# Optimization experiments

Measured on AMD Instinct MI355X. Metric: run time of the kernel, lower is better.

The kernel has to match this reference:

```python
import jax, jax.numpy as jnp
import numpy as np

B, N, R, E = 4, 50000, 100000, 1_600_000   # batch, nodes (wavelets_col), wavelets_row, nnz
D_IN, H1, H2, D_OUT = 32, 32, 16, 1
NEG_SLOPE = 0.2


def _xavier(k, shape):
    lim = float(np.sqrt(6.0 / (shape[0] + shape[1])))
    return jax.random.uniform(k, shape, jnp.float32, -lim, lim)


def setup_inputs() -> dict:
    key = jax.random.key(0)
    ks = jax.random.split(key, 16)
    # wavelets: sparse (R x N); inverse wavelets: sparse (N x R)
    w_rows = jax.random.randint(ks[0], (E,), 0, R)
    w_cols = jax.random.randint(ks[1], (E,), 0, N)
    wi_rows = jax.random.randint(ks[2], (E,), 0, N)
    wi_cols = jax.random.randint(ks[3], (E,), 0, R)
    return {
        "wavelets_indices": jnp.stack([w_rows, w_cols]),
        "wavelets_values": jax.random.normal(ks[4], (E,), jnp.float32) * 0.05,
        "wavelets_inverse_indices": jnp.stack([wi_rows, wi_cols]),
        "wavelets_inverse_values": jax.random.normal(ks[5], (E,), jnp.float32) * 0.05,
        "x_features": jax.random.normal(ks[6], (B, N, D_IN), jnp.float32),
        "W1": _xavier(ks[7], (D_IN, H1)),
        "diag1": 0.9 + 0.2 * jax.random.uniform(ks[8], (R,), jnp.float32),
        "W2": _xavier(ks[9], (H1, H2)),
        "diag2": 0.9 + 0.2 * jax.random.uniform(ks[10], (R,), jnp.float32),
        "reg_co_w": _xavier(ks[11], (H2, D_OUT)),
        "reg_co_b": jnp.zeros((D_OUT,), jnp.float32),
        "reg_co2_w": _xavier(ks[12], (H2, D_OUT)),
        "reg_co2_b": jnp.zeros((D_OUT,), jnp.float32),
    }


def _gw_layer(x, W, diag, w_idx, w_val, wi_idx, wi_val):
    # filtered = X @ W  -> (B, N, d)
    h = jnp.einsum("bnd,de->bne", x, W)
    d = W.shape[1]
    # T = wavelets (R x N) @ h  : scatter-add of gathered edge messages
    msg = h[:, w_idx[1], :] * w_val[None, :, None]          # (B, E, d)
    t = jnp.zeros((x.shape[0], R, d), h.dtype).at[:, w_idx[0], :].add(msg)
    # out = (wavelets_inverse * diag) (N x R) @ T  (diag rescales columns)
    coef = wi_val * diag[wi_idx[1]]                         # (E,)
    msg2 = t[:, wi_idx[1], :] * coef[None, :, None]         # (B, E, d)
    out = jnp.zeros((x.shape[0], N, d), h.dtype).at[:, wi_idx[0], :].add(msg2)
    return jax.nn.leaky_relu(out, NEG_SLOPE)                # dropout p=0.0 -> identity


def reference(wavelets_indices, wavelets_values, wavelets_inverse_indices,
              wavelets_inverse_values, x_features, W1, diag1, W2, diag2,
              reg_co_w, reg_co_b, reg_co2_w, reg_co2_b):
    x = _gw_layer(x_features, W1, diag1, wavelets_indices, wavelets_values,
                  wavelets_inverse_indices, wavelets_inverse_values)
    x = _gw_layer(x, W2, diag2, wavelets_indices, wavelets_values,
                  wavelets_inverse_indices, wavelets_inverse_values)
    co = x[:, -2, :] @ reg_co_w + reg_co_b                  # (B, 1)
    co2 = x[:, -1, :] @ reg_co2_w + reg_co2_b               # (B, 1)
    return jnp.concatenate([co[:, None, :], co2[:, None, :]], axis=1)  # (B, 2, 1)
```

## Files before the change

### kernel.cpp

```cpp
#include <hip/hip_runtime.h>

#define NEG_SLOPE 0.2f

static const int B = 4, N = 50000, R = 100000, E = 1600000;
static const int X2_CAP = 4096;
static const int R2_CAP = 4096;
static const int N1_CAP = 4096;
static const int RS_CAP = 49152;
static const int WDEG  = 64;
static const int WIDEG = 96;
static const int RBW = 3200;
static const int NBW = 1600;
static const int ZWORDS = RS_CAP + N1_CAP + RBW + NBW + 8;

__global__ void scanA(const int4* __restrict__ wi_rows4, const int4* __restrict__ wi_cols4,
                      const float4* __restrict__ wi_val4,
                      unsigned* __restrict__ bitsRS, int* __restrict__ rslot,
                      int2* __restrict__ x2list, int* __restrict__ tails, int e4) {
    int i = blockIdx.x * blockDim.x + threadIdx.x;
    if (i >= e4) return;
    int4 r = wi_rows4[i];
    int rr[4] = {r.x, r.y, r.z, r.w};
    bool any = false;
#pragma unroll
    for (int j = 0; j < 4; ++j) any = any || (rr[j] >= N - 2);
    if (!any) return;
    int4 c = wi_cols4[i];
    float4 v = wi_val4[i];
    int cc[4] = {c.x, c.y, c.z, c.w};
    float vv[4] = {v.x, v.y, v.z, v.w};
#pragma unroll
    for (int j = 0; j < 4; ++j) {
        if (rr[j] >= N - 2) {
            int col = cc[j];
            unsigned m = 1u << (col & 31);
            unsigned old = atomicOr(&bitsRS[col >> 5], m);
            if (!(old & m)) {
                int s = atomicAdd(&tails[3], 1);
                if (s < RS_CAP) rslot[col] = s;
            }
            int q = atomicAdd(&tails[0], 1);
            if (q < X2_CAP)
                x2list[q] = make_int2(col * 2 + (rr[j] - (N - 2)),
                                      __float_as_int(vv[j]));
        }
    }
}

__global__ void scanB(const int4* __restrict__ w_rows4, const int4* __restrict__ w_cols4,
                      const unsigned* __restrict__ bitsRS, unsigned* __restrict__ bitsN1,
                      int* __restrict__ n1slot, int* __restrict__ tails, int e4) {
    __shared__ int lcount, gbase;
    __shared__ int buf[1024];
    if (threadIdx.x == 0) {
        lcount = 0;
        if (blockIdx.x == 0) tails[4] = tails[3];
    }
    __syncthreads();
    int lane = threadIdx.x & 63;
    int i = blockIdx.x * blockDim.x + threadIdx.x;
    int4 r = make_int4(-1, -1, -1, -1);
    if (i < e4) r = w_rows4[i];
    int rr[4] = {r.x, r.y, r.z, r.w};
    unsigned fb[4];
#pragma unroll
    for (int j = 0; j < 4; ++j)
        fb[j] = (rr[j] >= 0) ? ((bitsRS[rr[j] >> 5] >> (rr[j] & 31)) & 1u) : 0u;
    bool anyf = (fb[0] | fb[1] | fb[2] | fb[3]) != 0u;
    int4 c = make_int4(0, 0, 0, 0);
    if (anyf) c = w_cols4[i];
    int cc[4] = {c.x, c.y, c.z, c.w};
#pragma unroll
    for (int j = 0; j < 4; ++j) {
        bool isnew = false;
        int n = 0;
        if (fb[j]) {
            n = cc[j];
            unsigned m = 1u << (n & 31);
            unsigned old = atomicOr(&bitsN1[n >> 5], m);
            isnew = (old & m) == 0u;
        }
        unsigned long long mb = __ballot(isnew);
        if (mb) {
            int leader = __ffsll(mb) - 1;
            int b0 = 0;
            if (lane == leader) b0 = atomicAdd(&lcount, __popcll(mb));
            b0 = __shfl(b0, leader);
            if (isnew) {
                int p = b0 + __popcll(mb & ((1ull << lane) - 1));
                if (p < 1024) buf[p] = n;
            }
        }
    }
    __syncthreads();
    int lc = lcount; if (lc > 1024) lc = 1024;
    if (threadIdx.x == 0 && lc > 0) gbase = atomicAdd(&tails[2], lc);
    __syncthreads();
    for (int t = threadIdx.x; t < lc; t += blockDim.x) {
        int slot = gbase + t;
        if (slot < N1_CAP) n1slot[buf[t]] = slot;
    }
}

__global__ void scanC(const int4* __restrict__ wi_rows4, const int4* __restrict__ wi_cols4,
                      const float4* __restrict__ wi_val4, const float* __restrict__ diag1,
                      const unsigned* __restrict__ bitsN1, const int* __restrict__ n1slot,
                      unsigned* __restrict__ bitsRS, int* __restrict__ rslot,
                      int* __restrict__ wi_cntC, int2* __restrict__ wi_pairs,
                      int* __restrict__ tails, int e4) {
    __shared__ int lcount, gbase;
    __shared__ int buf[1024];
    if (threadIdx.x == 0) lcount = 0;
    __syncthreads();
    int lane = threadIdx.x & 63;
    int i = blockIdx.x * blockDim.x + threadIdx.x;
    int4 r = make_int4(-1, -1, -1, -1);
    if (i < e4) r = wi_rows4[i];
    int rr[4] = {r.x, r.y, r.z, r.w};
    unsigned fb[4];
#pragma unroll
    for (int j = 0; j < 4; ++j)
        fb[j] = (rr[j] >= 0) ? ((bitsN1[rr[j] >> 5] >> (rr[j] & 31)) & 1u) : 0u;
    bool anyf = (fb[0] | fb[1] | fb[2] | fb[3]) != 0u;
    int4 c = make_int4(0, 0, 0, 0);
    float4 v = make_float4(0.f, 0.f, 0.f, 0.f);
    if (anyf) { c = wi_cols4[i]; v = wi_val4[i]; }
    int cc[4] = {c.x, c.y, c.z, c.w};
    float vv[4] = {v.x, v.y, v.z, v.w};
#pragma unroll
    for (int j = 0; j < 4; ++j) {
        bool isnew = false;
        int col = 0;
        if (fb[j]) {
            col = cc[j];
            float cf = vv[j] * diag1[col];
            int slot = n1slot[rr[j]];
            if (slot >= 0 && slot < N1_CAP) {
                int pos = atomicAdd(&wi_cntC[slot], 1);
                if (pos < WIDEG)
                    wi_pairs[(size_t)slot * WIDEG + pos] =
                        make_int2(col, __float_as_int(cf));
            }
            unsigned m = 1u << (col & 31);
            unsigned old = atomicOr(&bitsRS[col >> 5], m);
            isnew = (old & m) == 0u;
        }
        unsigned long long mb = __ballot(isnew);
        if (mb) {
            int leader = __ffsll(mb) - 1;
            int b0 = 0;
            if (lane == leader) b0 = atomicAdd(&lcount, __popcll(mb));
            b0 = __shfl(b0, leader);
            if (isnew) {
                int p = b0 + __popcll(mb & ((1ull << lane) - 1));
                if (p < 1024) buf[p] = col;
            }
        }
    }
    __syncthreads();
    int lc = lcount; if (lc > 1024) lc = 1024;
    if (threadIdx.x == 0 && lc > 0) gbase = atomicAdd(&tails[3], lc);
    __syncthreads();
    for (int t = threadIdx.x; t < lc; t += blockDim.x) {
        int s = gbase + t;
        if (s < RS_CAP) rslot[buf[t]] = s;
    }
}

__global__ void scanD(const int4* __restrict__ w_rows4, const int4* __restrict__ w_cols4,
                      const float4* __restrict__ w_val4,
                      const unsigned* __restrict__ bitsRS, const int* __restrict__ rslot,
                      int* __restrict__ w_cntC, int2* __restrict__ w_pairs, int e4) {
    int i = blockIdx.x * blockDim.x + threadIdx.x;
    if (i >= e4) return;
    int4 r = w_rows4[i];
    int rr[4] = {r.x, r.y, r.z, r.w};
    unsigned fb[4];
#pragma unroll
    for (int j = 0; j < 4; ++j) fb[j] = (bitsRS[rr[j] >> 5] >> (rr[j] & 31)) & 1u;
    if (!(fb[0] | fb[1] | fb[2] | fb[3])) return;
    int4 c = w_cols4[i];
    float4 v = w_val4[i];
    int cc[4] = {c.x, c.y, c.z, c.w};
    float vv[4] = {v.x, v.y, v.z, v.w};
    int s[4];
#pragma unroll
    for (int j = 0; j < 4; ++j) s[j] = fb[j] ? rslot[rr[j]] : RS_CAP;
#pragma unroll
    for (int j = 0; j < 4; ++j) {
        if (fb[j] && s[j] >= 0 && s[j] < RS_CAP) {
            int pos = atomicAdd(&w_cntC[s[j]], 1);
            if (pos < WDEG)
                w_pairs[(size_t)s[j] * WDEG + pos] =
                    make_int2(cc[j], __float_as_int(vv[j]));
        }
    }
}

__global__ void gather_t1(const float* __restrict__ x, float* __restrict__ t1C,
                          const int* __restrict__ w_cntC, const int2* __restrict__ w_pairs,
                          const int* __restrict__ tails) {
    int tot = tails[3]; if (tot > RS_CAP) tot = RS_CAP;
    int total = tot * 32;
    int gstride = gridDim.x * blockDim.x;
    for (int idx = blockIdx.x * blockDim.x + threadIdx.x; idx < total; idx += gstride) {
        int s = idx >> 5;
        int rem = idx & 31;
        int c4 = rem & 7;
        int b = rem >> 3;
        int L = w_cntC[s]; if (L > WDEG) L = WDEG;
        const int2* pr = w_pairs + (size_t)s * WDEG;
        const float4* sb = (const float4*)x + (size_t)b * N * 8 + c4;
        float4 acc = make_float4(0.f, 0.f, 0.f, 0.f);
        int i = 0;
        int L4 = L & ~3;
        for (; i < L4; i += 4) {
            int2 p0 = pr[i + 0];
            int2 p1 = pr[i + 1];
            int2 p2 = pr[i + 2];
            int2 p3 = pr[i + 3];
            float4 s0 = sb[(size_t)p0.x * 8];
            float4 s1 = sb[(size_t)p1.x * 8];
            float4 s2 = sb[(size_t)p2.x * 8];
            float4 s3 = sb[(size_t)p3.x * 8];
            float v0 = __int_as_float(p0.y), v1 = __int_as_float(p1.y);
            float v2 = __int_as_float(p2.y), v3 = __int_as_float(p3.y);
            acc.x += v0 * s0.x + v1 * s1.x + v2 * s2.x + v3 * s3.x;
            acc.y += v0 * s0.y + v1 * s1.y + v2 * s2.y + v3 * s3.y;
            acc.z += v0 * s0.z + v1 * s1.z + v2 * s2.z + v3 * s3.z;
            acc.w += v0 * s0.w + v1 * s1.w + v2 * s2.w + v3 * s3.w;
        }
        for (; i < L; ++i) {
            int2 p = pr[i];
            float4 sv = sb[(size_t)p.x * 8];
            float v = __int_as_float(p.y);
            acc.x += v * sv.x; acc.y += v * sv.y; acc.z += v * sv.z; acc.w += v * sv.w;
        }
        ((float4*)t1C)[(size_t)s * 32 + b * 8 + c4] = acc;
    }
}

__global__ void __launch_bounds__(256) x1mlp(
        const float* __restrict__ W1, const float* __restrict__ W2,
        const int* __restrict__ tails,
        const int* __restrict__ wi_cntC, const int2* __restrict__ wi_pairs,
        const int* __restrict__ rslot, const float* __restrict__ t1C,
        float* __restrict__ h2C) {
    __shared__ float W1s[1024], W2s[512];
    __shared__ float uls[8][128];
    __shared__ float ufin[128], x1ls[128];
    for (int i = threadIdx.x; i < 1024; i += 256) W1s[i] = W1[i];
    for (int i = threadIdx.x; i < 512; i += 256) W2s[i] = W2[i];
    int n1c = tails[2]; if (n1c > N1_CAP) n1c = N1_CAP;
    int g = threadIdx.x >> 5, t32 = threadIdx.x & 31;
    int b = t32 >> 3, c4 = t32 & 7;
    const float4* t1f4 = (const float4*)t1C;
    for (int s = blockIdx.x; s < n1c; s += gridDim.x) {
        int L = wi_cntC[s]; if (L > WIDEG) L = WIDEG;
        const int2* wip = wi_pairs + (size_t)s * WIDEG;
        float4 acc = make_float4(0.f, 0.f, 0.f, 0.f);
        for (int e = g; e < L; e += 8) {
            int2 pe = wip[e];
            int rs = rslot[pe.x];
            float coef = __int_as_float(pe.y);
            if (rs >= 0 && rs < RS_CAP) {
                float4 tv = t1f4[(size_t)rs * 32 + b * 8 + c4];
                acc.x += coef * tv.x; acc.y += coef * tv.y;
                acc.z += coef * tv.z; acc.w += coef * tv.w;
            }
        }
        float* up = &uls[g][b * 32 + c4 * 4];
        up[0] = acc.x; up[1] = acc.y; up[2] = acc.z; up[3] = acc.w;
        __syncthreads();
        if (threadIdx.x < 128) {
            float sum = 0.f;
#pragma unroll
            for (int gg = 0; gg < 8; ++gg) sum += uls[gg][threadIdx.x];
            ufin[threadIdx.x] = sum;
        }
        __syncthreads();
        if (threadIdx.x < 128) {
            int bb = threadIdx.x >> 5, c = threadIdx.x & 31;
            const float* ur = &ufin[bb * 32];
            float o = 0.f;
#pragma unroll
            for (int k = 0; k < 32; ++k) o += ur[k] * W1s[k * 32 + c];
            x1ls[threadIdx.x] = o > 0.f ? o : NEG_SLOPE * o;
        }
        __syncthreads();
        if (threadIdx.x < 64) {
            int bb = threadIdx.x >> 4, c = threadIdx.x & 15;
            const float* xr = &x1ls[bb * 32];
            float o = 0.f;
#pragma unroll
            for (int k = 0; k < 32; ++k) o += xr[k] * W2s[k * 16 + c];
            h2C[(size_t)s * 64 + bb * 16 + c] = o;
        }
        __syncthreads();
    }
}

__global__ void t2x2heads(const float* __restrict__ h2C,
                          const int* __restrict__ w_cntC, const int2* __restrict__ w_pairs,
                          const int* __restrict__ n1slot, const int* __restrict__ rslot,
                          const int* __restrict__ tails, float* __restrict__ t2C,
                          const int2* __restrict__ x2list,
                          const float* __restrict__ diag2,
                          const float* __restrict__ rw1, const float* __restrict__ rb1,
                          const float* __restrict__ rw2, const float* __restrict__ rb2,
                          float* __restrict__ out) {
    int r2c = tails[4]; if (r2c > R2_CAP) r2c = R2_CAP;
    for (int idx = threadIdx.x; idx < r2c * 16; idx += blockDim.x) {
        int s = idx >> 4;
        int rem = idx & 15;
        int c4 = rem & 3;
        int b = rem >> 2;
        int L = w_cntC[s]; if (L > WDEG) L = WDEG;
        const int2* pr = w_pairs + (size_t)s * WDEG;
        const float4* sb = (const float4*)h2C + b * 4 + c4;
        float4 acc = make_float4(0.f, 0.f, 0.f, 0.f);
        for (int i = 0; i < L; ++i) {
            int2 p = pr[i];
            int hs = n1slot[p.x];
            float v = __int_as_float(p.y);
            if (hs >= 0 && hs < N1_CAP) {
                float4 sv = sb[(size_t)hs * 16];
                acc.x += v * sv.x; acc.y += v * sv.y; acc.z += v * sv.z; acc.w += v * sv.w;
            }
        }
        ((float4*)t2C)[(size_t)s * 16 + b * 4 + c4] = acc;
    }
    __syncthreads();

    int cnt = tails[0]; if (cnt > X2_CAP) cnt = X2_CAP;
    int g = threadIdx.x >> 6, l = threadIdx.x & 63;
    int b = l >> 4, c = l & 15;
    float a0 = 0.f, a1 = 0.f;
    for (int i = g; i < cnt; i += 16) {
        int2 rec = x2list[i];
        int col = rec.x >> 1;
        int s = rslot[col];
        float coef = __int_as_float(rec.y) * diag2[col];
        float v = (s >= 0 && s < R2_CAP) ? t2C[(size_t)s * 64 + b * 16 + c] * coef : 0.f;
        if (rec.x & 1) a1 += v; else a0 += v;
    }
    __shared__ float red0[16][64], red1[16][64], xs[2][64];
    red0[g][l] = a0; red1[g][l] = a1;
    __syncthreads();
    if (threadIdx.x < 64) {
        float s0 = 0.f, s1 = 0.f;
#pragma unroll
        for (int gg = 0; gg < 16; ++gg) { s0 += red0[gg][threadIdx.x]; s1 += red1[gg][threadIdx.x]; }
        xs[0][threadIdx.x] = s0; xs[1][threadIdx.x] = s1;
    }
    __syncthreads();
    if (threadIdx.x < 8) {
        int bb = threadIdx.x >> 1, which = threadIdx.x & 1;
        const float* w = which ? rw2 : rw1;
        float acc = which ? rb2[0] : rb1[0];
        for (int k = 0; k < 16; ++k) {
            float xv = xs[which][bb * 16 + k];
            xv = xv > 0.f ? xv : NEG_SLOPE * xv;
            acc += xv * w[k];
        }
        out[bb * 2 + which] = acc;
    }
}

extern "C" void kernel_launch(void* const* d_in, const int* in_sizes, int n_in,
                              void* d_out, int out_size, void* d_ws, size_t ws_size,
                              hipStream_t stream) {
    const int*   w_rows  = (const int*)d_in[0];
    const int*   w_cols  = ((const int*)d_in[0]) + E;
    const float* w_val   = (const float*)d_in[1];
    const int*   wi_rows = (const int*)d_in[2];
    const int*   wi_cols = ((const int*)d_in[2]) + E;
    const float* wi_val  = (const float*)d_in[3];
    const float* x       = (const float*)d_in[4];
    const float* W1      = (const float*)d_in[5];
    const float* diag1   = (const float*)d_in[6];
    const float* W2      = (const float*)d_in[7];
    const float* diag2   = (const float*)d_in[8];
    const float* rw1     = (const float*)d_in[9];
    const float* rb1     = (const float*)d_in[10];
    const float* rw2     = (const float*)d_in[11];
    const float* rb2     = (const float*)d_in[12];
    float* out = (float*)d_out;

    float* t1C = (float*)d_ws;
    float* h2C = t1C + (size_t)RS_CAP * 128;
    float* t2C = h2C + (size_t)N1_CAP * 64;
    int* ip = (int*)(t2C + (size_t)R2_CAP * 64);
    int* w_cntC  = ip; ip += RS_CAP;
    int* wi_cntC = ip; ip += N1_CAP;
    unsigned* bitsRS = (unsigned*)ip; ip += RBW;
    unsigned* bitsN1 = (unsigned*)ip; ip += NBW;
    int* tails = ip; ip += 8;
    int* rslot  = ip; ip += R;
    int* n1slot = ip; ip += N;
    int2* x2list = (int2*)ip; ip += 2 * X2_CAP;
    int2* w_pairs  = (int2*)ip; ip += 2 * (size_t)RS_CAP * WDEG;
    int2* wi_pairs = (int2*)ip; ip += 2 * (size_t)N1_CAP * WIDEG;

    const int e4 = E / 4;
    const int blk = 256;
    const int scanGrid = (e4 + blk - 1) / blk;

    (void)hipMemsetAsync(w_cntC, 0, (size_t)ZWORDS * sizeof(int), stream);

    scanA<<<scanGrid, blk, 0, stream>>>((const int4*)wi_rows, (const int4*)wi_cols,
                                        (const float4*)wi_val, bitsRS, rslot,
                                        x2list, tails, e4);
    scanB<<<scanGrid, blk, 0, stream>>>((const int4*)w_rows, (const int4*)w_cols,
                                        bitsRS, bitsN1, n1slot, tails, e4);
    scanC<<<scanGrid, blk, 0, stream>>>((const int4*)wi_rows, (const int4*)wi_cols,
                                        (const float4*)wi_val, diag1, bitsN1, n1slot,
                                        bitsRS, rslot, wi_cntC, wi_pairs, tails, e4);
    scanD<<<scanGrid, blk, 0, stream>>>((const int4*)w_rows, (const int4*)w_cols,
                                        (const float4*)w_val, bitsRS, rslot,
                                        w_cntC, w_pairs, e4);
    gather_t1<<<2048, blk, 0, stream>>>(x, t1C, w_cntC, w_pairs, tails);
    x1mlp<<<1024, blk, 0, stream>>>(W1, W2, tails, wi_cntC, wi_pairs, rslot, t1C, h2C);
    t2x2heads<<<1, 1024, 0, stream>>>(h2C, w_cntC, w_pairs, n1slot, rslot, tails,
                                      t2C, x2list, diag2, rw1, rb1, rw2, rb2, out);
}
```

Before: 260.6 us.

## Split single-block t2 gather into multi-block kernel with edge-parallel reduction

```diff
diff --git a/kernel.cpp b/kernel.cpp
--- a/kernel.cpp
+++ b/kernel.cpp
@@ -300,38 +300,55 @@
     }
 }
 
-__global__ void t2x2heads(const float* __restrict__ h2C,
-                          const int* __restrict__ w_cntC, const int2* __restrict__ w_pairs,
-                          const int* __restrict__ n1slot, const int* __restrict__ rslot,
-                          const int* __restrict__ tails, float* __restrict__ t2C,
-                          const int2* __restrict__ x2list,
-                          const float* __restrict__ diag2,
-                          const float* __restrict__ rw1, const float* __restrict__ rb1,
-                          const float* __restrict__ rw2, const float* __restrict__ rb2,
-                          float* __restrict__ out) {
+__global__ void __launch_bounds__(256) t2gather(
+        const float* __restrict__ h2C,
+        const int* __restrict__ w_cntC, const int2* __restrict__ w_pairs,
+        const int* __restrict__ n1slot, const int* __restrict__ tails,
+        float* __restrict__ t2C) {
+    __shared__ float4 red[16][16];
     int r2c = tails[4]; if (r2c > R2_CAP) r2c = R2_CAP;
-    for (int idx = threadIdx.x; idx < r2c * 16; idx += blockDim.x) {
-        int s = idx >> 4;
-        int rem = idx & 15;
-        int c4 = rem & 3;
-        int b = rem >> 2;
+    int e0 = threadIdx.x >> 4;
+    int l  = threadIdx.x & 15;
+    int b = l >> 2, c4 = l & 3;
+    const float4* sb = (const float4*)h2C + b * 4 + c4;
+    for (int s = blockIdx.x; s < r2c; s += gridDim.x) {
         int L = w_cntC[s]; if (L > WDEG) L = WDEG;
         const int2* pr = w_pairs + (size_t)s * WDEG;
-        const float4* sb = (const float4*)h2C + b * 4 + c4;
         float4 acc = make_float4(0.f, 0.f, 0.f, 0.f);
-        for (int i = 0; i < L; ++i) {
+        for (int i = e0; i < L; i += 16) {
             int2 p = pr[i];
             int hs = n1slot[p.x];
             float v = __int_as_float(p.y);
             if (hs >= 0 && hs < N1_CAP) {
                 float4 sv = sb[(size_t)hs * 16];
-                acc.x += v * sv.x; acc.y += v * sv.y; acc.z += v * sv.z; acc.w += v * sv.w;
-            }
-        }
-        ((float4*)t2C)[(size_t)s * 16 + b * 4 + c4] = acc;
-    }
-    __syncthreads();
-
+                acc.x += v * sv.x; acc.y += v * sv.y;
+                acc.z += v * sv.z; acc.w += v * sv.w;
+            }
+        }
+        red[e0][l] = acc;
+        __syncthreads();
+#pragma unroll
+        for (int off = 8; off >= 1; off >>= 1) {
+            if (e0 < off) {
+                float4 o = red[e0 + off][l];
+                float4 a = red[e0][l];
+                a.x += o.x; a.y += o.y; a.z += o.z; a.w += o.w;
+                red[e0][l] = a;
+            }
+            __syncthreads();
+        }
+        if (e0 == 0)
+            ((float4*)t2C)[(size_t)s * 16 + l] = red[0][l];
+        __syncthreads();
+    }
+}
+
+__global__ void heads(const int* __restrict__ rslot, const int* __restrict__ tails,
+                      const float* __restrict__ t2C, const int2* __restrict__ x2list,
+                      const float* __restrict__ diag2,
+                      const float* __restrict__ rw1, const float* __restrict__ rb1,
+                      const float* __restrict__ rw2, const float* __restrict__ rb2,
+                      float* __restrict__ out) {
     int cnt = tails[0]; if (cnt > X2_CAP) cnt = X2_CAP;
     int g = threadIdx.x >> 6, l = threadIdx.x & 63;
     int b = l >> 4, c = l & 15;
@@ -421,6 +438,7 @@
                                         w_cntC, w_pairs, e4);
     gather_t1<<<2048, blk, 0, stream>>>(x, t1C, w_cntC, w_pairs, tails);
     x1mlp<<<1024, blk, 0, stream>>>(W1, W2, tails, wi_cntC, wi_pairs, rslot, t1C, h2C);
-    t2x2heads<<<1, 1024, 0, stream>>>(h2C, w_cntC, w_pairs, n1slot, rslot, tails,
-                                      t2C, x2list, diag2, rw1, rb1, rw2, rb2, out);
-}
+    t2gather<<<128, blk, 0, stream>>>(h2C, w_cntC, w_pairs, n1slot, tails, t2C);
+    heads<<<1, 1024, 0, stream>>>(rslot, tails, t2C, x2list, diag2,
+                                  rw1, rb1, rw2, rb2, out);
+}
```

After: 241.9 us. 7.2% less time.
